# Optimization experiments

Measured on AMD Instinct MI355X. Metric: run time of the kernel, lower is better.

Reference implementation:

```python
import jax, jax.numpy as jnp
import numpy as np

N, E, H, EF = 50000, 800000, 128, 32
MSG_IN = 2 * H + EF + 3  # 291
UPD_IN = 2 * H           # 256


def _mlp(x, W1, b1, W2, b2):
    # Linear -> ReLU -> Linear (act=True: ReLU between layers)
    h = jax.nn.relu(x @ W1 + b1)
    return h @ W2 + b2


def _layernorm(x, gamma, beta, eps=1e-5):
    mu = jnp.mean(x, axis=-1, keepdims=True)
    var = jnp.var(x, axis=-1, keepdims=True)
    return (x - mu) * jax.lax.rsqrt(var + eps) * gamma + beta


def setup_inputs() -> dict:
    key = jax.random.key(0)
    ks = jax.random.split(key, 12)
    def w(k, shape):
        fan_in = shape[0]
        return jax.random.uniform(k, shape, jnp.float32, -1.0, 1.0) / np.sqrt(fan_in)
    return {
        "x": jax.random.normal(ks[0], (N, H), jnp.float32),
        "edge_index": jax.random.randint(ks[1], (2, E), 0, N, jnp.int32),
        "edge_attr": jax.random.normal(ks[2], (E, EF), jnp.float32),
        "coords": jax.random.normal(ks[3], (N, 3), jnp.float32),
        "mW1": w(ks[4], (MSG_IN, H)), "mb1": jnp.zeros((H,), jnp.float32),
        "mW2": w(ks[5], (H, H)),      "mb2": jnp.zeros((H,), jnp.float32),
        "uW1": w(ks[6], (UPD_IN, H)), "ub1": jnp.zeros((H,), jnp.float32),
        "uW2": w(ks[7], (H, H)),      "ub2": jnp.zeros((H,), jnp.float32),
        "gamma": jnp.ones((H,), jnp.float32),
        "beta": jnp.zeros((H,), jnp.float32),
    }


def reference(x, edge_index, edge_attr, coords,
              mW1, mb1, mW2, mb2, uW1, ub1, uW2, ub2, gamma, beta):
    src, dst = edge_index[0], edge_index[1]
    rel_coords = coords[dst] - coords[src]                       # (E, 3)
    msg_input = jnp.concatenate([x[src], x[dst], edge_attr, rel_coords], axis=-1)  # (E, MSG_IN)
    messages = _mlp(msg_input, mW1, mb1, mW2, mb2)               # (E, H)
    aggr = jax.ops.segment_sum(messages, dst, num_segments=x.shape[0])  # (N, H)
    update_input = jnp.concatenate([x, aggr], axis=-1)           # (N, 2H)
    out = _mlp(update_input, uW1, ub1, uW2, ub2)                 # (N, H)
    return _layernorm(x + out, gamma, beta)
```

## Files before the change

### kernel.cpp

```cpp
#include <hip/hip_runtime.h>

#define NN 50000
#define NE 800000
#define HD 128

typedef short short8 __attribute__((ext_vector_type(8)));
typedef float floatx4 __attribute__((ext_vector_type(4)));
typedef float floatx16 __attribute__((ext_vector_type(16)));

static __device__ __forceinline__ unsigned short f2bf(float f) {
    unsigned int u = __float_as_uint(f);
    unsigned int lsb = (u >> 16) & 1u;
    u += 0x7fffu + lsb;
    return (unsigned short)(u >> 16);
}

static __device__ __forceinline__ short8 pack2(float4 a, float4 b) {
    union { unsigned int u[4]; short8 s; } r;
    asm("v_cvt_pk_bf16_f32 %0, %1, %2" : "=v"(r.u[0]) : "v"(a.x), "v"(a.y));
    asm("v_cvt_pk_bf16_f32 %0, %1, %2" : "=v"(r.u[1]) : "v"(a.z), "v"(a.w));
    asm("v_cvt_pk_bf16_f32 %0, %1, %2" : "=v"(r.u[2]) : "v"(b.x), "v"(b.y));
    asm("v_cvt_pk_bf16_f32 %0, %1, %2" : "=v"(r.u[3]) : "v"(b.z), "v"(b.w));
    return r.s;
}

static __device__ __forceinline__ floatx4 mfma16x16x32(short8 a, short8 b, floatx4 c) {
    asm("v_mfma_f32_16x16x32_bf16 %0, %1, %2, %0" : "+v"(c) : "v"(a), "v"(b));
    return c;
}

static __device__ __forceinline__ floatx16 mfma32x32x16(short8 a, short8 b, floatx16 c) {
    asm("v_mfma_f32_32x32x16_bf16 %0, %1, %2, %0" : "+v"(c) : "v"(a), "v"(b));
    return c;
}

#define NOPGUARD_INIT8(A) asm volatile("s_nop 3" \
  : "+v"(A[0]),"+v"(A[1]),"+v"(A[2]),"+v"(A[3]),"+v"(A[4]),"+v"(A[5]),"+v"(A[6]),"+v"(A[7]))
#define NOPGUARD8(A) asm volatile("s_nop 7\ns_nop 7" \
  : "+v"(A[0]),"+v"(A[1]),"+v"(A[2]),"+v"(A[3]),"+v"(A[4]),"+v"(A[5]),"+v"(A[6]),"+v"(A[7]))
#define NOPGUARD_INIT4x16(A) asm volatile("s_nop 7" \
  : "+v"(A[0]),"+v"(A[1]),"+v"(A[2]),"+v"(A[3]))
#define NOPGUARD4x16(A) asm volatile("s_nop 7\ns_nop 7\ns_nop 7" \
  : "+v"(A[0]),"+v"(A[1]),"+v"(A[2]),"+v"(A[3]))

#define WAVE_LDS_FENCE() asm volatile("s_waitcnt lgkmcnt(0)" ::: "memory")

__global__ void pack_weights(const float* __restrict__ mW1, const float* __restrict__ mW2,
                             const float* __restrict__ uW1, const float* __restrict__ uW2,
                             unsigned short* __restrict__ W1q, unsigned short* __restrict__ W2q,
                             unsigned short* __restrict__ U1p, unsigned short* __restrict__ U2p) {
    int t = blockIdx.x * 256 + threadIdx.x;
    if (t < 40960) {
        int i = t;
        int j = i & 7, lane = (i >> 3) & 63, n = (i >> 9) & 3, s = i >> 11;
        int k = s * 16 + ((lane >> 5) << 3) + j;
        int c = n * 32 + (lane & 31);
        W1q[i] = f2bf((k < 291) ? mW1[k * 128 + c] : 0.0f);
    } else if (t < 57344) {
        int i = t - 40960;
        int j = i & 7, lane = (i >> 3) & 63, n = (i >> 9) & 3, s = i >> 11;
        int k = s * 16 + ((lane >> 5) << 3) + j;
        int c = n * 32 + (lane & 31);
        W2q[i] = f2bf(mW2[k * 128 + c]);
    } else if (t < 90112) {
        int i = t - 57344;
        int j = i & 7, lane = (i >> 3) & 63, n = (i >> 9) & 7, kk = i >> 12;
        int k = kk * 32 + ((lane >> 4) << 3) + j;
        int c = n * 16 + (lane & 15);
        U1p[i] = f2bf(uW1[k * 128 + c]);
    } else if (t < 106496) {
        int i = t - 90112;
        int j = i & 7, lane = (i >> 3) & 63, n = (i >> 9) & 7, kk = i >> 12;
        int k = kk * 32 + ((lane >> 4) << 3) + j;
        int c = n * 16 + (lane & 15);
        U2p[i] = f2bf(uW2[k * 128 + c]);
    }
}

__global__ void cast_kernel(const float* __restrict__ in, unsigned short* __restrict__ out,
                            int n8) {
    int t = blockIdx.x * 256 + threadIdx.x;
    if (t < n8) {
        float4 a = *reinterpret_cast<const float4*>(in + (size_t)t * 8);
        float4 b = *reinterpret_cast<const float4*>(in + (size_t)t * 8 + 4);
        *reinterpret_cast<short8*>(out + (size_t)t * 8) = pack2(a, b);
    }
}

__global__ void hist_kernel(const int* __restrict__ ei, int* __restrict__ counts) {
    int e = blockIdx.x * 256 + threadIdx.x;
    if (e < NE) atomicAdd(&counts[ei[NE + e]], 1);
}

__global__ __launch_bounds__(1024)
void scan1_kernel(const int* __restrict__ counts, int* __restrict__ partial,
                  int* __restrict__ bsum) {
    __shared__ int wsum[16];
    int tid = threadIdx.x;
    int gid = blockIdx.x * 1024 + tid;
    int lane = tid & 63, w = tid >> 6;
    int v = (gid < NN) ? counts[gid] : 0;
    int s = v;
    #pragma unroll
    for (int o = 1; o < 64; o <<= 1) { int t = __shfl_up(s, o); if (lane >= o) s += t; }
    if (lane == 63) wsum[w] = s;
    __syncthreads();
    if (w == 0 && lane < 16) {
        int t = wsum[lane];
        #pragma unroll
        for (int o = 1; o < 16; o <<= 1) { int u = __shfl_up(t, o); if (lane >= o) t += u; }
        wsum[lane] = t;
    }
    __syncthreads();
    int base = (w > 0) ? wsum[w - 1] : 0;
    if (gid < NN) partial[gid] = base + s - v;
    if (tid == 1023) bsum[blockIdx.x] = base + s;
}

__global__ void scan2_kernel(int* __restrict__ bsum, int n) {
    int lane = threadIdx.x;
    int v = (lane < n) ? bsum[lane] : 0;
    int s = v;
    #pragma unroll
    for (int o = 1; o < 64; o <<= 1) { int t = __shfl_up(s, o); if (lane >= o) s += t; }
    if (lane < n) bsum[lane] = s - v;
}

__global__ void scatter_kernel(const int* __restrict__ ei, const int* __restrict__ partial,
                               const int* __restrict__ bsum, int* __restrict__ cursor,
                               const float* __restrict__ cd, const float* __restrict__ ea,
                               unsigned int* __restrict__ epack,
                               uint2* __restrict__ relb,
                               unsigned short* __restrict__ eab) {
    int e = blockIdx.x * 256 + threadIdx.x;
    if (e < NE) {
        int d = ei[NE + e];
        int s = ei[e];
        int pos = partial[d] + bsum[d >> 10] + atomicAdd(&cursor[d], 1);
        epack[pos] = (unsigned int)s | ((unsigned int)d << 16);
        float r0 = cd[d * 3 + 0] - cd[s * 3 + 0];
        float r1 = cd[d * 3 + 1] - cd[s * 3 + 1];
        float r2 = cd[d * 3 + 2] - cd[s * 3 + 2];
        uint2 rr;
        asm("v_cvt_pk_bf16_f32 %0, %1, %2" : "=v"(rr.x) : "v"(r0), "v"(r1));
        asm("v_cvt_pk_bf16_f32 %0, %1, %2" : "=v"(rr.y) : "v"(r2), "v"(0.0f));
        relb[pos] = rr;
        const float* eap = ea + (size_t)e * 32;
        unsigned short* eo = eab + (size_t)pos * 32;
        #pragma unroll
        for (int q = 0; q < 4; ++q) {
            float4 a = *reinterpret_cast<const float4*>(eap + q * 8);
            float4 b = *reinterpret_cast<const float4*>(eap + q * 8 + 4);
            *reinterpret_cast<short8*>(eo + q * 8) = pack2(a, b);
        }
    }
}

__global__ __launch_bounds__(256, 4)
void msg_kernel(const unsigned short* __restrict__ xb, const unsigned short* __restrict__ eab,
                const unsigned int* __restrict__ epack, const uint2* __restrict__ relb,
                const unsigned short* __restrict__ W1q, const float* __restrict__ mb1,
                const float* __restrict__ mb2,
                float* __restrict__ aggr) {
    __shared__ unsigned short sH[128 * 136];
    __shared__ unsigned short sW[2048];
    __shared__ int sDst[128];

    const int tid = threadIdx.x;
    const int lane = tid & 63;
    const int wid = tid >> 6;
    const int lr31 = lane & 31;
    const int half = lane >> 5;
    const int wrow = wid * 32 + lr31;
    const int eidx = blockIdx.x * 128 + wrow;

    const unsigned int p = epack[eidx];
    const int src = (int)(p & 0xFFFFu);
    const int dst = (int)(p >> 16);
    if (half == 0) sDst[wrow] = dst;

    const unsigned short* xs = xb + (size_t)src * 128 + half * 8;
    const unsigned short* xd = xb + (size_t)dst * 128 + half * 8;
    const unsigned short* epr = eab + (size_t)eidx * 32 + half * 8;
    const uint2 rr = relb[eidx];

    short8 wpre = *reinterpret_cast<const short8*>(W1q + tid * 8);

    floatx16 acc[4];
    #pragma unroll
    for (int n = 0; n < 4; ++n)
        #pragma unroll
        for (int q = 0; q < 16; ++q) acc[n][q] = 0.0f;
    NOPGUARD_INIT4x16(acc);

    #pragma unroll
    for (int s = 0; s < 19; ++s) {
        *reinterpret_cast<short8*>(sW + tid * 8) = wpre;
        __syncthreads();
        {
            int nc = (s < 18) ? (s + 1) * 2048 : 40960;
            wpre = *reinterpret_cast<const short8*>(W1q + nc + tid * 8);
        }
        short8 a;
        if (s < 8) {
            a = *reinterpret_cast<const short8*>(xs + s * 16);
        } else if (s < 16) {
            a = *reinterpret_cast<const short8*>(xd + (s - 8) * 16);
        } else if (s < 18) {
            a = *reinterpret_cast<const short8*>(epr + (s - 16) * 16);
        } else {
            union { unsigned int u[4]; short8 s8; } a9;
            a9.u[0] = (half == 0) ? rr.x : 0u;
            a9.u[1] = (half == 0) ? rr.y : 0u;
            a9.u[2] = 0u; a9.u[3] = 0u;
            a = a9.s8;
        }
        #pragma unroll
        for (int n = 0; n < 4; ++n) {
            short8 b = *reinterpret_cast<const short8*>(sW + n * 512 + lane * 8);
            acc[n] = mfma32x32x16(a, b, acc[n]);
        }
        __syncthreads();
    }
    NOPGUARD4x16(acc);

    unsigned int hm32;
    {
        bool head = false;
        if (lane < 32) {
            int r = wid * 32 + lane;
            head = (lane == 0) || (sDst[r] != sDst[r - 1]);
        }
        unsigned long long m = __ballot(head);
        hm32 = (unsigned int)(m & 0xFFFFFFFFull);
    }

    #pragma unroll
    for (int n = 0; n < 4; ++n) {
        float bias = mb1[n * 32 + lr31];
        #pragma unroll
        for (int q = 0; q < 16; ++q) {
            int crow = (q & 3) + 8 * (q >> 2) + 4 * half;
            sH[(wid * 32 + crow) * 136 + n * 32 + lr31] = f2bf(fmaxf(acc[n][q] + bias, 0.0f));
        }
    }
    WAVE_LDS_FENCE();

    floatx16 acc2[4];
    #pragma unroll
    for (int n = 0; n < 4; ++n)
        #pragma unroll
        for (int q = 0; q < 16; ++q) acc2[n][q] = 0.0f;
    NOPGUARD_INIT4x16(acc2);

    #pragma unroll
    for (int s = 0; s < 8; ++s) {
        *reinterpret_cast<short8*>(sW + tid * 8) = wpre;
        __syncthreads();
        if (s < 7)
            wpre = *reinterpret_cast<const short8*>(W1q + 40960 + (s + 1) * 2048 + tid * 8);
        short8 a = *reinterpret_cast<const short8*>(&sH[wrow * 136 + s * 16 + half * 8]);
        #pragma unroll
        for (int n = 0; n < 4; ++n) {
            short8 b = *reinterpret_cast<const short8*>(sW + n * 512 + lane * 8);
            acc2[n] = mfma32x32x16(a, b, acc2[n]);
        }
        __syncthreads();
    }
    NOPGUARD4x16(acc2);
    WAVE_LDS_FENCE();

    #pragma unroll
    for (int n = 0; n < 4; ++n) {
        float bias = mb2[n * 32 + lr31];
        #pragma unroll
        for (int q = 0; q < 16; ++q) {
            int crow = (q & 3) + 8 * (q >> 2) + 4 * half;
            sH[(wid * 32 + crow) * 136 + n * 32 + lr31] = f2bf(acc2[n][q] + bias);
        }
    }
    WAVE_LDS_FENCE();

    {
        unsigned int m = hm32;
        while (m) {
            int start = __ffs(m) - 1;
            unsigned int m2 = m & (m - 1);
            int end = m2 ? (__ffs(m2) - 1) : 32;
            float sum0 = 0.0f, sum1 = 0.0f;
            for (int r = start; r < end; ++r) {
                int rw = wid * 32 + r;
                unsigned int u0 = sH[rw * 136 + lane];
                unsigned int u1 = sH[rw * 136 + 64 + lane];
                sum0 += __uint_as_float(u0 << 16);
                sum1 += __uint_as_float(u1 << 16);
            }
            int d = sDst[wid * 32 + start];
            atomicAdd(&aggr[d * 128 + lane], sum0);
            atomicAdd(&aggr[d * 128 + 64 + lane], sum1);
            m = m2;
        }
    }
}

__global__
void node_kernel(const unsigned short* __restrict__ xb, const float* __restrict__ x,
                 const float* __restrict__ aggr,
                 const unsigned short* __restrict__ U1p, const float* __restrict__ ub1,
                 const unsigned short* __restrict__ U2p, const float* __restrict__ ub2,
                 const float* __restrict__ gamma, const float* __restrict__ beta,
                 float* __restrict__ out) {
    __shared__ unsigned short sH[64 * 136];

    const int tid = threadIdx.x;
    const int lane = tid & 63;
    const int wid = tid >> 6;
    const int g = lane >> 4;
    const int lr = lane & 15;
    const int arow = wid * 16 + lr;
    const int n0 = blockIdx.x * 64;

    int nd0 = n0 + arow;
    int ndc0 = (nd0 < NN) ? nd0 : (NN - 1);

    const unsigned short* xp = xb + (size_t)ndc0 * 128 + g * 8;
    const float* ap = aggr + (size_t)ndc0 * 128 + g * 8;

    short8 af[8];
    float4 ta[8];
    #pragma unroll
    for (int kk = 0; kk < 4; ++kk) {
        af[kk] = *reinterpret_cast<const short8*>(xp + kk * 32);
        ta[2 * kk]     = *reinterpret_cast<const float4*>(ap + kk * 32);
        ta[2 * kk + 1] = *reinterpret_cast<const float4*>(ap + kk * 32 + 4);
    }
    #pragma unroll
    for (int kk = 0; kk < 4; ++kk)
        af[4 + kk] = pack2(ta[2 * kk], ta[2 * kk + 1]);

    floatx4 acc[8];
    #pragma unroll
    for (int n = 0; n < 8; ++n)
        #pragma unroll
        for (int r = 0; r < 4; ++r) acc[n][r] = 0.0f;
    NOPGUARD_INIT8(acc);

    #pragma unroll
    for (int kk = 0; kk < 8; ++kk) {
        const short8* wb = reinterpret_cast<const short8*>(U1p) + (kk * 8) * 64 + lane;
        #pragma unroll
        for (int n = 0; n < 8; ++n)
            acc[n] = mfma16x16x32(af[kk], wb[n * 64], acc[n]);
    }
    NOPGUARD8(acc);

    #pragma unroll
    for (int n = 0; n < 8; ++n) {
        float bias = ub1[n * 16 + lr];
        #pragma unroll
        for (int r = 0; r < 4; ++r) {
            int row = wid * 16 + g * 4 + r;
            sH[row * 136 + n * 16 + lr] = f2bf(fmaxf(acc[n][r] + bias, 0.0f));
        }
    }
    WAVE_LDS_FENCE();

    short8 a2[4];
    #pragma unroll
    for (int kk = 0; kk < 4; ++kk)
        a2[kk] = *reinterpret_cast<const short8*>(&sH[arow * 136 + kk * 32 + g * 8]);

    floatx4 acc2[8];
    #pragma unroll
    for (int n = 0; n < 8; ++n)
        #pragma unroll
        for (int r = 0; r < 4; ++r) acc2[n][r] = 0.0f;
    NOPGUARD_INIT8(acc2);

    #pragma unroll
    for (int kk = 0; kk < 4; ++kk) {
        const short8* wb = reinterpret_cast<const short8*>(U2p) + (kk * 8) * 64 + lane;
        #pragma unroll
        for (int n = 0; n < 8; ++n)
            acc2[n] = mfma16x16x32(a2[kk], wb[n * 64], acc2[n]);
    }
    NOPGUARD8(acc2);

    #pragma unroll
    for (int r = 0; r < 4; ++r) {
        int row = wid * 16 + g * 4 + r;
        int nd = n0 + row;
        int ndc = (nd < NN) ? nd : (NN - 1);
        float vals[8];
        float s1 = 0.0f, s2 = 0.0f;
        #pragma unroll
        for (int n = 0; n < 8; ++n) {
            int col = n * 16 + lr;
            float v = acc2[n][r] + ub2[col] + x[ndc * 128 + col];
            vals[n] = v;
            s1 += v;
            s2 += v * v;
        }
        #pragma unroll
        for (int m = 1; m < 16; m <<= 1) {
            s1 += __shfl_xor(s1, m);
            s2 += __shfl_xor(s2, m);
        }
        float mean = s1 * (1.0f / 128.0f);
        float var = s2 * (1.0f / 128.0f) - mean * mean;
        float inv = rsqrtf(var + 1e-5f);
        if (nd < NN) {
            #pragma unroll
            for (int n = 0; n < 8; ++n) {
                int col = n * 16 + lr;
                out[nd * 128 + col] = (vals[n] - mean) * inv * gamma[col] + beta[col];
            }
        }
    }
}

extern "C" void kernel_launch(void* const* d_in, const int* in_sizes, int n_in,
                              void* d_out, int out_size, void* d_ws, size_t ws_size,
                              hipStream_t stream) {
    const float* x     = (const float*)d_in[0];
    const int*   ei    = (const int*)d_in[1];
    const float* ea    = (const float*)d_in[2];
    const float* cd    = (const float*)d_in[3];
    const float* mW1   = (const float*)d_in[4];
    const float* mb1   = (const float*)d_in[5];
    const float* mW2   = (const float*)d_in[6];
    const float* mb2   = (const float*)d_in[7];
    const float* uW1   = (const float*)d_in[8];
    const float* ub1   = (const float*)d_in[9];
    const float* uW2   = (const float*)d_in[10];
    const float* ub2   = (const float*)d_in[11];
    const float* gamma = (const float*)d_in[12];
    const float* beta  = (const float*)d_in[13];
    float* out = (float*)d_out;

    char* ws = (char*)d_ws;
    unsigned short* W1q = (unsigned short*)(ws);
    unsigned short* W2q = (unsigned short*)(ws + 81920);
    unsigned short* U1p = (unsigned short*)(ws + 114688);
    unsigned short* U2p = (unsigned short*)(ws + 180224);
    int* counts  = (int*)(ws + 212992);
    int* cursor  = (int*)(ws + 413696);
    int* partial = (int*)(ws + 614400);
    int* bsum    = (int*)(ws + 815104);
    unsigned int* epack = (unsigned int*)(ws + 815360);
    uint2* relb  = (uint2*)(ws + 4015360);
    unsigned short* xbuf = (unsigned short*)(ws + 10415360);
    unsigned short* eabuf = (unsigned short*)(ws + 23215360);

    float* aggr = out;

    hipMemsetAsync(counts, 0, (size_t)(614400 - 212992), stream);
    hipMemsetAsync(aggr, 0, (size_t)NN * HD * sizeof(float), stream);

    pack_weights<<<416, 256, 0, stream>>>(mW1, mW2, uW1, uW2, W1q, W2q, U1p, U2p);
    cast_kernel<<<(NN * HD / 8 + 255) / 256, 256, 0, stream>>>(x, xbuf, NN * HD / 8);
    hist_kernel<<<(NE + 255) / 256, 256, 0, stream>>>(ei, counts);
    scan1_kernel<<<(NN + 1023) / 1024, 1024, 0, stream>>>(counts, partial, bsum);
    scan2_kernel<<<1, 64, 0, stream>>>(bsum, (NN + 1023) / 1024);
    scatter_kernel<<<(NE + 255) / 256, 256, 0, stream>>>(ei, partial, bsum, cursor, cd, ea, epack, relb, eabuf);
    msg_kernel<<<NE / 128, 256, 0, stream>>>(xbuf, eabuf, epack, relb, W1q, mb1, mb2, aggr);
    node_kernel<<<(NN + 63) / 64, 256, 0, stream>>>(xbuf, x, aggr, U1p, ub1, U2p, ub2, gamma, beta, out);
}
```

Baseline: 313.4 us.

## Fuse x/edge_attr casting and histogram into one prep kernel, gather edge_attr by id

Merges the x cast, the dst histogram and the edge_attr bf16 cast into a single prep kernel, so the edge_attr conversion becomes a coalesced linear pass instead of a scatter to sorted positions inside scatter_kernel. The sorted edge record grows to 64 bits and now carries the original edge id, which msg_kernel uses to gather edge_attr rows in original order. This cuts a launch and makes the scatter lighter, at the cost of a larger epack read and uncoalesced edge_attr reads in msg_kernel.

```diff
diff --git a/kernel.cpp b/kernel.cpp
--- a/kernel.cpp
+++ b/kernel.cpp
@@ -77,19 +77,21 @@
     }
 }
 
-__global__ void cast_kernel(const float* __restrict__ in, unsigned short* __restrict__ out,
-                            int n8) {
+__global__ void prep_kernel(const float* __restrict__ x, unsigned short* __restrict__ xbuf,
+                            const float* __restrict__ ea, unsigned short* __restrict__ eabuf,
+                            const int* __restrict__ ei, int* __restrict__ counts) {
     int t = blockIdx.x * 256 + threadIdx.x;
-    if (t < n8) {
-        float4 a = *reinterpret_cast<const float4*>(in + (size_t)t * 8);
-        float4 b = *reinterpret_cast<const float4*>(in + (size_t)t * 8 + 4);
-        *reinterpret_cast<short8*>(out + (size_t)t * 8) = pack2(a, b);
-    }
-}
-
-__global__ void hist_kernel(const int* __restrict__ ei, int* __restrict__ counts) {
-    int e = blockIdx.x * 256 + threadIdx.x;
-    if (e < NE) atomicAdd(&counts[ei[NE + e]], 1);
+    if (t < 800000) {
+        float4 a = *reinterpret_cast<const float4*>(x + (size_t)t * 8);
+        float4 b = *reinterpret_cast<const float4*>(x + (size_t)t * 8 + 4);
+        *reinterpret_cast<short8*>(xbuf + (size_t)t * 8) = pack2(a, b);
+        atomicAdd(&counts[ei[NE + t]], 1);
+    } else if (t < 4000000) {
+        int u = t - 800000;
+        float4 a = *reinterpret_cast<const float4*>(ea + (size_t)u * 8);
+        float4 b = *reinterpret_cast<const float4*>(ea + (size_t)u * 8 + 4);
+        *reinterpret_cast<short8*>(eabuf + (size_t)u * 8) = pack2(a, b);
+    }
 }
 
 __global__ __launch_bounds__(1024)
@@ -128,16 +130,17 @@
 
 __global__ void scatter_kernel(const int* __restrict__ ei, const int* __restrict__ partial,
                                const int* __restrict__ bsum, int* __restrict__ cursor,
-                               const float* __restrict__ cd, const float* __restrict__ ea,
-                               unsigned int* __restrict__ epack,
-                               uint2* __restrict__ relb,
-                               unsigned short* __restrict__ eab) {
+                               const float* __restrict__ cd,
+                               unsigned long long* __restrict__ epack,
+                               uint2* __restrict__ relb) {
     int e = blockIdx.x * 256 + threadIdx.x;
     if (e < NE) {
         int d = ei[NE + e];
         int s = ei[e];
         int pos = partial[d] + bsum[d >> 10] + atomicAdd(&cursor[d], 1);
-        epack[pos] = (unsigned int)s | ((unsigned int)d << 16);
+        epack[pos] = (unsigned long long)e
+                   | ((unsigned long long)s << 20)
+                   | ((unsigned long long)d << 36);
         float r0 = cd[d * 3 + 0] - cd[s * 3 + 0];
         float r1 = cd[d * 3 + 1] - cd[s * 3 + 1];
         float r2 = cd[d * 3 + 2] - cd[s * 3 + 2];
@@ -145,20 +148,12 @@
         asm("v_cvt_pk_bf16_f32 %0, %1, %2" : "=v"(rr.x) : "v"(r0), "v"(r1));
         asm("v_cvt_pk_bf16_f32 %0, %1, %2" : "=v"(rr.y) : "v"(r2), "v"(0.0f));
         relb[pos] = rr;
-        const float* eap = ea + (size_t)e * 32;
-        unsigned short* eo = eab + (size_t)pos * 32;
-        #pragma unroll
-        for (int q = 0; q < 4; ++q) {
-            float4 a = *reinterpret_cast<const float4*>(eap + q * 8);
-            float4 b = *reinterpret_cast<const float4*>(eap + q * 8 + 4);
-            *reinterpret_cast<short8*>(eo + q * 8) = pack2(a, b);
-        }
     }
 }
 
 __global__ __launch_bounds__(256, 4)
 void msg_kernel(const unsigned short* __restrict__ xb, const unsigned short* __restrict__ eab,
-                const unsigned int* __restrict__ epack, const uint2* __restrict__ relb,
+                const unsigned long long* __restrict__ epack, const uint2* __restrict__ relb,
                 const unsigned short* __restrict__ W1q, const float* __restrict__ mb1,
                 const float* __restrict__ mb2,
                 float* __restrict__ aggr) {
@@ -174,14 +169,15 @@
     const int wrow = wid * 32 + lr31;
     const int eidx = blockIdx.x * 128 + wrow;
 
-    const unsigned int p = epack[eidx];
-    const int src = (int)(p & 0xFFFFu);
-    const int dst = (int)(p >> 16);
+    const unsigned long long p = epack[eidx];
+    const int eid = (int)(p & 0xFFFFFull);
+    const int src = (int)((p >> 20) & 0xFFFFull);
+    const int dst = (int)(p >> 36);
     if (half == 0) sDst[wrow] = dst;
 
     const unsigned short* xs = xb + (size_t)src * 128 + half * 8;
     const unsigned short* xd = xb + (size_t)dst * 128 + half * 8;
-    const unsigned short* epr = eab + (size_t)eidx * 32 + half * 8;
+    const unsigned short* epr = eab + (size_t)eid * 32 + half * 8;
     const uint2 rr = relb[eidx];
 
     short8 wpre = *reinterpret_cast<const short8*>(W1q + tid * 8);
@@ -447,10 +443,10 @@
     int* cursor  = (int*)(ws + 413696);
     int* partial = (int*)(ws + 614400);
     int* bsum    = (int*)(ws + 815104);
-    unsigned int* epack = (unsigned int*)(ws + 815360);
-    uint2* relb  = (uint2*)(ws + 4015360);
-    unsigned short* xbuf = (unsigned short*)(ws + 10415360);
-    unsigned short* eabuf = (unsigned short*)(ws + 23215360);
+    unsigned long long* epack = (unsigned long long*)(ws + 815360);
+    uint2* relb  = (uint2*)(ws + 7215360);
+    unsigned short* xbuf = (unsigned short*)(ws + 13615360);
+    unsigned short* eabuf = (unsigned short*)(ws + 26415360);
 
     float* aggr = out;
 
@@ -458,11 +454,10 @@
     hipMemsetAsync(aggr, 0, (size_t)NN * HD * sizeof(float), stream);
 
     pack_weights<<<416, 256, 0, stream>>>(mW1, mW2, uW1, uW2, W1q, W2q, U1p, U2p);
-    cast_kernel<<<(NN * HD / 8 + 255) / 256, 256, 0, stream>>>(x, xbuf, NN * HD / 8);
-    hist_kernel<<<(NE + 255) / 256, 256, 0, stream>>>(ei, counts);
+    prep_kernel<<<(4000000 + 255) / 256, 256, 0, stream>>>(x, xbuf, ea, eabuf, ei, counts);
     scan1_kernel<<<(NN + 1023) / 1024, 1024, 0, stream>>>(counts, partial, bsum);
     scan2_kernel<<<1, 64, 0, stream>>>(bsum, (NN + 1023) / 1024);
-    scatter_kernel<<<(NE + 255) / 256, 256, 0, stream>>>(ei, partial, bsum, cursor, cd, ea, epack, relb, eabuf);
+    scatter_kernel<<<(NE + 255) / 256, 256, 0, stream>>>(ei, partial, bsum, cursor, cd, epack, relb);
     msg_kernel<<<NE / 128, 256, 0, stream>>>(xbuf, eabuf, epack, relb, W1q, mb1, mb2, aggr);
     node_kernel<<<(NN + 63) / 64, 256, 0, stream>>>(xbuf, x, aggr, U1p, ub1, U2p, ub2, gamma, beta, out);
 }
```

Result: faster. 276.9 us (-11.6%).
